# Kernel optimization log

Measured on AMD Instinct MI355X. Metric: run time of the kernel, lower is better.

## Reference

```python
import jax, jax.numpy as jnp
import numpy as np

D = 1024
H = 16
HD = D // H  # 64
LN_EPS = 1e-5


def _layernorm(x, w, b):
    m = jnp.mean(x, axis=-1, keepdims=True)
    v = jnp.mean(jnp.square(x - m), axis=-1, keepdims=True)
    return (x - m) * jax.lax.rsqrt(v + LN_EPS) * w + b


def _attention(x, w_qkv, b_qkv, w_proj, b_proj):
    # x: [B, S, D]. Block-diagonal mask == attention within each sequence,
    # so batched per-sequence attention is exactly equivalent to packed fmha.
    B, S, _ = x.shape
    qkv = x @ w_qkv + b_qkv                      # [B, S, 3D]
    q, k, v = jnp.split(qkv, 3, axis=-1)
    q = q.reshape(B, S, H, HD)
    k = k.reshape(B, S, H, HD)
    v = v.reshape(B, S, H, HD)
    scale = 1.0 / jnp.sqrt(jnp.asarray(HD, dtype=x.dtype))
    scores = jnp.einsum('bqhd,bkhd->bhqk', q, k) * scale  # [B, H, S, S]
    probs = jax.nn.softmax(scores, axis=-1)
    out = jnp.einsum('bhqk,bkhd->bqhd', probs, v).reshape(B, S, D)
    return out @ w_proj + b_proj


def _block(x, w_qkv, b_qkv, w_proj, b_proj, ln1_w, ln1_b,
           w_fc1, b_fc1, w_fc2, b_fc2, ln2_w, ln2_b, gamma1, gamma2):
    # x = x + ls1(attn(norm1(x)))
    x = x + gamma1 * _attention(_layernorm(x, ln1_w, ln1_b), w_qkv, b_qkv, w_proj, b_proj)
    # x = x + ls2(mlp(norm2(x)))
    h = _layernorm(x, ln2_w, ln2_b)
    h = jax.nn.gelu(h @ w_fc1 + b_fc1, approximate=False) @ w_fc2 + b_fc2
    return x + gamma2 * h


def setup_inputs() -> dict:
    key = jax.random.key(0)
    ks = jax.random.split(key, 8)
    s = 0.02
    return {
        'x1': jax.random.normal(ks[0], (8, 1024, D), jnp.float32),
        'x2': jax.random.normal(ks[1], (8, 512, D), jnp.float32),
        'w_qkv': jax.random.normal(ks[2], (D, 3 * D), jnp.float32) * s,
        'b_qkv': jnp.zeros((3 * D,), jnp.float32),
        'w_proj': jax.random.normal(ks[3], (D, D), jnp.float32) * s,
        'b_proj': jnp.zeros((D,), jnp.float32),
        'ln1_w': jnp.ones((D,), jnp.float32),
        'ln1_b': jnp.zeros((D,), jnp.float32),
        'ln2_w': jnp.ones((D,), jnp.float32),
        'ln2_b': jnp.zeros((D,), jnp.float32),
        'w_fc1': jax.random.normal(ks[4], (D, 4 * D), jnp.float32) * s,
        'b_fc1': jnp.zeros((4 * D,), jnp.float32),
        'w_fc2': jax.random.normal(ks[5], (4 * D, D), jnp.float32) * s,
        'b_fc2': jnp.zeros((D,), jnp.float32),
        'gamma1': jnp.full((D,), 1e-5, jnp.float32),  # LayerScale init_values
        'gamma2': jnp.full((D,), 1e-5, jnp.float32),
    }


def reference(x1, x2, w_qkv, b_qkv, w_proj, b_proj, ln1_w, ln1_b,
              ln2_w, ln2_b, w_fc1, b_fc1, w_fc2, b_fc2, gamma1, gamma2):
    params = (w_qkv, b_qkv, w_proj, b_proj, ln1_w, ln1_b,
              w_fc1, b_fc1, w_fc2, b_fc2, ln2_w, ln2_b, gamma1, gamma2)
    y1 = _block(x1, *params)
    y2 = _block(x2, *params)
    return (y1, y2)
```

## Files before the change

### kernel.cpp

```cpp
#include <hip/hip_runtime.h>
#include <cstddef>


typedef __bf16 b16x8 __attribute__((ext_vector_type(8)));
typedef float f32x4 __attribute__((ext_vector_type(4)));
typedef unsigned short u16x8 __attribute__((ext_vector_type(8)));
typedef unsigned short u16x4 __attribute__((ext_vector_type(4)));
typedef float f32x4v __attribute__((ext_vector_type(4)));

__device__ __forceinline__ unsigned short f2bf(float f) {
    unsigned int u = __builtin_bit_cast(unsigned int, f);
    return (unsigned short)((u + 0x7fffu + ((u >> 16) & 1u)) >> 16);
}
__device__ __forceinline__ unsigned short f2bf_trunc(float f) {
    return (unsigned short)(__builtin_bit_cast(unsigned int, f) >> 16);
}

__device__ __forceinline__ float exp2_f(float x) {
#if defined(__has_builtin)
#if __has_builtin(__builtin_amdgcn_exp2f)
    return __builtin_amdgcn_exp2f(x);
#else
    return exp2f(x);
#endif
#else
    return exp2f(x);
#endif
}

#define AS1C(p) ((const __attribute__((address_space(1))) void*)(p))
#define AS3(p)  ((__attribute__((address_space(3))) void*)(p))
#define FENCE() asm volatile("" ::: "memory")

__global__ __launch_bounds__(256) void wtrans_k(const float* __restrict__ in,
                                                unsigned short* __restrict__ out,
                                                int K, int N) {
    __shared__ float tile[32][33];
    int n0 = blockIdx.x << 5, k0 = blockIdx.y << 5;
    int tx = threadIdx.x & 31;
    int ty = threadIdx.x >> 5;
#pragma unroll
    for (int j = 0; j < 4; ++j)
        tile[ty + j * 8][tx] = in[(size_t)(k0 + ty + j * 8) * N + n0 + tx];
    __syncthreads();
#pragma unroll
    for (int j = 0; j < 4; ++j)
        out[(size_t)(n0 + ty + j * 8) * K + k0 + tx] = f2bf(tile[tx][ty + j * 8]);
}

__global__ __launch_bounds__(256) void vtrans_k(const unsigned short* __restrict__ qkv,
                                                unsigned short* __restrict__ vT) {
    __shared__ unsigned short tile[32][40];
    int tok0 = blockIdx.x << 5, c0 = blockIdx.y << 5;
    int tx = threadIdx.x & 31, ty = threadIdx.x >> 5;
#pragma unroll
    for (int j = 0; j < 4; ++j)
        tile[ty + j * 8][tx] = qkv[(size_t)(tok0 + ty + j * 8) * 3072 + 2048 + c0 + tx];
    __syncthreads();
#pragma unroll
    for (int j = 0; j < 4; ++j)
        vT[(size_t)(c0 + ty + j * 8) * 12288 + tok0 + tx] = tile[tx][ty + j * 8];
}

__global__ __launch_bounds__(256) void ln_k(const float* __restrict__ srcA,
                                            const float* __restrict__ srcB, int split,
                                            const float* __restrict__ w,
                                            const float* __restrict__ b,
                                            unsigned short* __restrict__ out) {
    int row = blockIdx.x;
    const float* src = (row < split) ? srcA + (size_t)row * 1024
                                     : srcB + (size_t)(row - split) * 1024;
    int t = threadIdx.x;
    f32x4v v = *(const f32x4v*)(src + t * 4);
    float s = v[0] + v[1] + v[2] + v[3];
    float s2 = v[0] * v[0] + v[1] * v[1] + v[2] * v[2] + v[3] * v[3];
#pragma unroll
    for (int off = 1; off < 64; off <<= 1) {
        s += __shfl_xor(s, off);
        s2 += __shfl_xor(s2, off);
    }
    __shared__ float red[8];
    int wv4 = t >> 6;
    if ((t & 63) == 0) { red[wv4 * 2] = s; red[wv4 * 2 + 1] = s2; }
    __syncthreads();
    s = red[0] + red[2] + red[4] + red[6];
    s2 = red[1] + red[3] + red[5] + red[7];
    float mean = s * (1.0f / 1024.0f);
    float var = s2 * (1.0f / 1024.0f) - mean * mean;
    float rstd = rsqrtf(var + 1e-5f);
    f32x4v wv = *(const f32x4v*)(w + t * 4);
    f32x4v bv = *(const f32x4v*)(b + t * 4);
    u16x4 ov;
#pragma unroll
    for (int j = 0; j < 4; ++j) ov[j] = f2bf((v[j] - mean) * rstd * wv[j] + bv[j]);
    *(u16x4*)(out + (size_t)row * 1024 + t * 4) = ov;
}

template <int BM, int K, int NN, int EPI>
__global__ __launch_bounds__(512, 1) void gemm3_k(
    const unsigned short* __restrict__ A, const unsigned short* __restrict__ BT,
    const float* __restrict__ bias, const float* __restrict__ scale,
    const float* __restrict__ rx1, const float* __restrict__ rx2,
    float* __restrict__ outf, unsigned short* __restrict__ outb) {
    constexpr int NT = K / 64;
    constexpr int ntn = NN >> 8;
    constexpr int GA = BM / 64;
    constexpr int NFR = BM / 32;
    constexpr int HALF = NFR / 2;
    constexpr int ABUF = BM * 128;
    constexpr int STRIDE = ABUF + 32768;
    __shared__ char lds[2 * STRIDE];
    const int t = threadIdx.x;
    const int lane = t & 63, w = t >> 6, lr = lane & 15, lg = lane >> 4;
    const int wm = w >> 2, wn = w & 3;
    const int nwg = gridDim.x;
    const int bid = blockIdx.x;
    const int swz = (bid & 7) * (nwg >> 3) + (bid >> 3);
    const int m0 = (swz / ntn) * BM;
    const int n0 = (swz % ntn) << 8;

    const int srow = t >> 3;
    const int scol = ((t & 7) ^ (srow & 7)) * 8;
    const unsigned short* ga = A + (size_t)(m0 + srow) * K + scol;
    const unsigned short* gb = BT + (size_t)(n0 + srow) * K + scol;

    f32x4 acc[NFR][4] = {};
    b16x8 af[HALF][2], b01[2][2], b23[2][2];

    auto ISSUE_A = [&](int tile, int g) {
        char* dst = lds + (tile & 1) * STRIDE + g * 8192 + t * 16;
        __builtin_amdgcn_global_load_lds(AS1C(ga + (size_t)(g * 64) * K + tile * 64),
                                         AS3(dst), 16, 0, 0);
    };
    auto ISSUE_B = [&](int tile, int g) {
        char* dst = lds + (tile & 1) * STRIDE + ABUF + g * 8192 + t * 16;
        __builtin_amdgcn_global_load_lds(AS1C(gb + (size_t)(g * 64) * K + tile * 64),
                                         AS3(dst), 16, 0, 0);
    };

    const int cs0 = (lg ^ (lr & 7)) * 16;
    const int cs1 = ((4 + lg) ^ (lr & 7)) * 16;

    auto RD_A = [&](const char* buf, int mg) {
#pragma unroll
        for (int mi = 0; mi < HALF; ++mi) {
            const char* p = buf + (wm * (BM / 2) + (mg + mi) * 16 + lr) * 128;
            af[mi][0] = *(const b16x8*)(p + cs0);
            af[mi][1] = *(const b16x8*)(p + cs1);
        }
    };
    auto RD_B = [&](const char* buf, b16x8 (*bf)[2], int ng) {
#pragma unroll
        for (int ni = 0; ni < 2; ++ni) {
            const char* p = buf + ABUF + (wn * 64 + (ng + ni) * 16 + lr) * 128;
            bf[ni][0] = *(const b16x8*)(p + cs0);
            bf[ni][1] = *(const b16x8*)(p + cs1);
        }
    };
    auto MM = [&](int mg, b16x8 (*bf)[2], int ng) {
        __builtin_amdgcn_s_setprio(1);
#pragma unroll
        for (int kk = 0; kk < 2; ++kk)
#pragma unroll
            for (int mi = 0; mi < HALF; ++mi)
#pragma unroll
                for (int ni = 0; ni < 2; ++ni)
                    acc[mg + mi][ng + ni] = __builtin_amdgcn_mfma_f32_16x16x32_bf16(
                        af[mi][kk], bf[ni][kk], acc[mg + mi][ng + ni], 0, 0, 0);
        __builtin_amdgcn_s_setprio(0);
    };
    auto WAIT_GA = [&]() {
        if constexpr (GA == 4) asm volatile("s_waitcnt vmcnt(4)" ::: "memory");
        else                   asm volatile("s_waitcnt vmcnt(3)" ::: "memory");
    };

#pragma unroll
    for (int g = 0; g < GA; ++g) ISSUE_A(0, g);
#pragma unroll
    for (int g = 0; g < 4; ++g) ISSUE_B(0, g);
#pragma unroll
    for (int g = 0; g < GA; ++g) ISSUE_A(1, g);
    WAIT_GA();
    __builtin_amdgcn_s_barrier();
    FENCE();

    for (int kt = 0; kt < NT; ++kt) {
        const char* buf = lds + (kt & 1) * STRIDE;
        RD_A(buf, 0); RD_B(buf, b01, 0);
        if (kt + 1 < NT) { ISSUE_B(kt + 1, 0); ISSUE_B(kt + 1, 1); }
        __builtin_amdgcn_s_barrier(); FENCE();
        MM(0, b01, 0);
        __builtin_amdgcn_s_barrier(); FENCE();
        RD_B(buf, b23, 2);
        if (kt + 1 < NT) { ISSUE_B(kt + 1, 2); ISSUE_B(kt + 1, 3); }
        __builtin_amdgcn_s_barrier(); FENCE();
        MM(0, b23, 2);
        __builtin_amdgcn_s_barrier(); FENCE();
        RD_A(buf, HALF);
        __builtin_amdgcn_s_barrier(); FENCE();
        MM(HALF, b23, 2);
        __builtin_amdgcn_s_barrier(); FENCE();
        if (kt + 2 < NT) {
#pragma unroll
            for (int g = 0; g < GA; ++g) ISSUE_A(kt + 2, g);
        }
        __builtin_amdgcn_s_barrier(); FENCE();
        MM(HALF, b01, 0);
        if (kt + 1 < NT) {
            if (kt + 2 < NT) WAIT_GA();
            else             asm volatile("s_waitcnt vmcnt(0)" ::: "memory");
            __builtin_amdgcn_s_barrier(); FENCE();
        }
    }

    if (EPI == 0 || EPI == 2) {
        __syncthreads();
        char* clb = lds;
        const int rl0 = wm * (BM / 2) + lg * 4;
        const int cl0 = wn * 64 + lr;
#pragma unroll
        for (int n = 0; n < 4; ++n) {
            const int col_l = cl0 + n * 16;
            const float bval = bias[n0 + col_l];
            const int colByte = col_l * 2;
            const int within = colByte & 15;
            const int chunk = colByte >> 4;
#pragma unroll
            for (int m = 0; m < NFR; ++m) {
#pragma unroll
                for (int r = 0; r < 4; ++r) {
                    float c = acc[m][n][r] + bval;
                    if (EPI == 2) {
                        float u = c * (c * c * 0.044715f + 1.0f) * 1.5957691216057308f;
                        c = c * __builtin_amdgcn_rcpf(1.0f + __expf(-u));
                    }
                    const int row_l = rl0 + m * 16 + r;
                    *(unsigned short*)(clb + row_l * 512 +
                                       (((chunk ^ (row_l & 7)) << 4) | within)) = f2bf(c);
                }
            }
        }
        __syncthreads();
#pragma unroll
        for (int it = 0; it < BM / 16; ++it) {
            int idx = it * 512 + t;
            int row = idx >> 5, ch = idx & 31;
            u16x8 v = *(const u16x8*)(clb + row * 512 + ((ch ^ (row & 7)) << 4));
            *(u16x8*)(outb + (size_t)(m0 + row) * NN + n0 + ch * 8) = v;
        }
    } else {
        const int rbase = m0 + wm * (BM / 2) + lg * 4;
        const int cbase = n0 + wn * 64 + lr;
#pragma unroll
        for (int n = 0; n < 4; ++n) {
            int col = cbase + n * 16;
            float bval = bias[col];
            float sval = scale[col];
#pragma unroll
            for (int m = 0; m < NFR; ++m) {
                int row = rbase + m * 16;
#pragma unroll
                for (int r = 0; r < 4; ++r) {
                    float c = acc[m][n][r] + bval;
                    size_t idx = (size_t)(row + r) * NN + col;
                    if (EPI == 1) {
                        float xv = (row + r < 8192) ? rx1[idx] : rx2[idx - (size_t)8192 * 1024];
                        outf[idx] = xv + sval * c;
                    } else {
                        outf[idx] += sval * c;
                    }
                }
            }
        }
    }
}

__global__ __launch_bounds__(512) void attn_k(const unsigned short* __restrict__ qkv,
                                              const unsigned short* __restrict__ vT,
                                              unsigned short* __restrict__ aout) {
    __shared__ char sK[2][8192];
    __shared__ char sV[2][8192];
    __shared__ unsigned short sP[8][16 * 72];
    int bid = (blockIdx.x & 7) * (gridDim.x >> 3) + (blockIdx.x >> 3);
    int t = threadIdx.x, lane = t & 63, w = t >> 6, lr = lane & 15, lg = lane >> 4;
    int seq0, S, h, qt;
    if (bid < 1024) {
        int b = bid >> 7, r = bid & 127;
        h = r >> 3; qt = r & 7; seq0 = b << 10; S = 1024;
    } else {
        int i2 = bid - 1024;
        int b = i2 >> 6, r = i2 & 63;
        h = r >> 2; qt = r & 3; seq0 = 8192 + (b << 9); S = 512;
    }
    int tok0 = seq0 + qt * 128;
    const size_t hoff = (size_t)h * 64;

    const int srow = t >> 3;
    const int sc = ((t & 7) ^ (srow & 7)) * 8;
    const unsigned short* kg = qkv + (size_t)(seq0 + srow) * 3072 + 1024 + hoff + sc;
    const unsigned short* vg = vT + (size_t)(hoff + srow) * 12288 + seq0 + sc;

    b16x8 aq0, aq1;
    {
        const unsigned short* qb = qkv + (size_t)(tok0 + w * 16 + lr) * 3072 + hoff;
        aq0 = *(const b16x8*)(qb + lg * 8);
        aq1 = *(const b16x8*)(qb + 32 + lg * 8);
    }

    auto STAGE = [&](int kt) {
        int slot = kt & 1;
        __builtin_amdgcn_global_load_lds(AS1C(kg + (size_t)(kt << 6) * 3072),
                                         AS3(sK[slot] + t * 16), 16, 0, 0);
        __builtin_amdgcn_global_load_lds(AS1C(vg + (kt << 6)),
                                         AS3(sV[slot] + t * 16), 16, 0, 0);
    };

    const int swz0 = (lg ^ (lr & 7)) * 16;
    const int swz1 = ((4 + lg) ^ (lr & 7)) * 16;
    const float SC = 0.18033688f;

    float m_run[4] = {-1e30f, -1e30f, -1e30f, -1e30f};
    float l_run[4] = {0.f, 0.f, 0.f, 0.f};
    f32x4 o[4] = {};
    unsigned short* sPw = sP[w];
    int nkv = S >> 6;

    STAGE(0);
    for (int kt = 0; kt < nkv; ++kt) {
        if (kt + 1 < nkv) {
            STAGE(kt + 1);
            asm volatile("s_waitcnt vmcnt(2)" ::: "memory");
        } else {
            asm volatile("s_waitcnt vmcnt(0)" ::: "memory");
        }
        __builtin_amdgcn_s_barrier();
        FENCE();
        const char* kb = sK[kt & 1];
        const char* vb = sV[kt & 1];
        f32x4 s[4];
#pragma unroll
        for (int n = 0; n < 4; ++n) {
            const char* kr = kb + (n * 16 + lr) * 128;
            b16x8 bk0 = *(const b16x8*)(kr + swz0);
            b16x8 bk1 = *(const b16x8*)(kr + swz1);
            f32x4 z = {};
            z = __builtin_amdgcn_mfma_f32_16x16x32_bf16(aq0, bk0, z, 0, 0, 0);
            z = __builtin_amdgcn_mfma_f32_16x16x32_bf16(aq1, bk1, z, 0, 0, 0);
            s[n] = z * SC;
        }
        float p[4][4];
#pragma unroll
        for (int r = 0; r < 4; ++r) {
            float tm = fmaxf(fmaxf(s[0][r], s[1][r]), fmaxf(s[2][r], s[3][r]));
            tm = fmaxf(tm, __shfl_xor(tm, 1));
            tm = fmaxf(tm, __shfl_xor(tm, 2));
            tm = fmaxf(tm, __shfl_xor(tm, 4));
            tm = fmaxf(tm, __shfl_xor(tm, 8));
            float mn = fmaxf(m_run[r], tm);
            float alpha = exp2_f(m_run[r] - mn);
            m_run[r] = mn;
            float rs = 0.f;
#pragma unroll
            for (int n = 0; n < 4; ++n) {
                float pv = exp2_f(s[n][r] - mn);
                p[n][r] = pv;
                rs += pv;
            }
            rs += __shfl_xor(rs, 1);
            rs += __shfl_xor(rs, 2);
            rs += __shfl_xor(rs, 4);
            rs += __shfl_xor(rs, 8);
            l_run[r] = l_run[r] * alpha + rs;
#pragma unroll
            for (int n = 0; n < 4; ++n) o[n][r] *= alpha;
        }
#pragma unroll
        for (int r = 0; r < 4; ++r)
#pragma unroll
            for (int n = 0; n < 4; ++n)
                sPw[(lg * 4 + r) * 72 + n * 16 + lr] = f2bf_trunc(p[n][r]);
        b16x8 ap0 = *(const b16x8*)(&sPw[lr * 72 + lg * 8]);
        b16x8 ap1 = *(const b16x8*)(&sPw[lr * 72 + 32 + lg * 8]);
#pragma unroll
        for (int n = 0; n < 4; ++n) {
            const char* vr = vb + (n * 16 + lr) * 128;
            b16x8 bv0 = *(const b16x8*)(vr + swz0);
            b16x8 bv1 = *(const b16x8*)(vr + swz1);
            o[n] = __builtin_amdgcn_mfma_f32_16x16x32_bf16(ap0, bv0, o[n], 0, 0, 0);
            o[n] = __builtin_amdgcn_mfma_f32_16x16x32_bf16(ap1, bv1, o[n], 0, 0, 0);
        }
        FENCE();
        if (kt + 1 < nkv) __builtin_amdgcn_s_barrier();
        FENCE();
    }
    __syncthreads();
    char* ob = sK[0];
#pragma unroll
    for (int r = 0; r < 4; ++r) {
        float inv = __builtin_amdgcn_rcpf(l_run[r]);
        const int row_l = w * 16 + lg * 4 + r;
#pragma unroll
        for (int n = 0; n < 4; ++n) {
            const int colByte = (n * 16 + lr) * 2;
            *(unsigned short*)(ob + row_l * 128 +
                               ((((colByte >> 4) ^ (row_l & 7)) << 4) | (colByte & 15))) =
                f2bf(o[n][r] * inv);
        }
    }
    __syncthreads();
#pragma unroll
    for (int it = 0; it < 2; ++it) {
        int idx = it * 512 + t;
        int row = idx >> 3, ch = idx & 7;
        u16x8 v = *(const u16x8*)(ob + row * 128 + ((ch ^ (row & 7)) << 4));
        *(u16x8*)(aout + (size_t)(tok0 + row) * 1024 + hoff + ch * 8) = v;
    }
}

extern "C" void kernel_launch(void* const* d_in, const int* in_sizes, int n_in,
                              void* d_out, int out_size, void* d_ws, size_t ws_size,
                              hipStream_t stream) {
    const float* x1     = (const float*)d_in[0];
    const float* x2     = (const float*)d_in[1];
    const float* w_qkv  = (const float*)d_in[2];
    const float* b_qkv  = (const float*)d_in[3];
    const float* w_proj = (const float*)d_in[4];
    const float* b_proj = (const float*)d_in[5];
    const float* ln1w   = (const float*)d_in[6];
    const float* ln1b   = (const float*)d_in[7];
    const float* ln2w   = (const float*)d_in[8];
    const float* ln2b   = (const float*)d_in[9];
    const float* w_fc1  = (const float*)d_in[10];
    const float* b_fc1  = (const float*)d_in[11];
    const float* w_fc2  = (const float*)d_in[12];
    const float* b_fc2  = (const float*)d_in[13];
    const float* gamma1 = (const float*)d_in[14];
    const float* gamma2 = (const float*)d_in[15];
    float* out = (float*)d_out;
    char* ws = (char*)d_ws;

    unsigned short* wqkvT  = (unsigned short*)(ws);
    unsigned short* wprojT = (unsigned short*)(ws + 6291456);
    unsigned short* wfc1T  = (unsigned short*)(ws + 8388608);
    unsigned short* wfc2T  = (unsigned short*)(ws + 16777216);
    unsigned short* lnbuf  = (unsigned short*)(ws + 25165824);
    unsigned short* qkvbuf = (unsigned short*)(ws + 50331648);
    unsigned short* attnbuf= (unsigned short*)(ws + 125829120);
    unsigned short* actbuf = (unsigned short*)(ws + 50331648);
    unsigned short* vTbuf  = lnbuf;

    wtrans_k<<<dim3(96, 32), 256, 0, stream>>>(w_qkv, wqkvT, 1024, 3072);
    wtrans_k<<<dim3(32, 32), 256, 0, stream>>>(w_proj, wprojT, 1024, 1024);
    wtrans_k<<<dim3(128, 32), 256, 0, stream>>>(w_fc1, wfc1T, 1024, 4096);
    wtrans_k<<<dim3(32, 128), 256, 0, stream>>>(w_fc2, wfc2T, 4096, 1024);
    ln_k<<<12288, 256, 0, stream>>>(x1, x2, 8192, ln1w, ln1b, lnbuf);
    gemm3_k<192, 1024, 3072, 0><<<768, 512, 0, stream>>>(lnbuf, wqkvT, b_qkv, nullptr,
                                                         nullptr, nullptr, nullptr, qkvbuf);
    vtrans_k<<<dim3(384, 32), 256, 0, stream>>>(qkvbuf, vTbuf);
    attn_k<<<1536, 512, 0, stream>>>(qkvbuf, vTbuf, attnbuf);
    gemm3_k<192, 1024, 1024, 1><<<256, 512, 0, stream>>>(attnbuf, wprojT, b_proj, gamma1,
                                                         x1, x2, out, nullptr);
    ln_k<<<12288, 256, 0, stream>>>(out, out + (size_t)8192 * 1024, 8192, ln2w, ln2b, lnbuf);
    gemm3_k<256, 1024, 4096, 2><<<768, 512, 0, stream>>>(lnbuf, wfc1T, b_fc1, nullptr,
                                                         nullptr, nullptr, nullptr, actbuf);
    gemm3_k<192, 4096, 1024, 3><<<256, 512, 0, stream>>>(actbuf, wfc2T, b_fc2, gamma2,
                                                         nullptr, nullptr, out, nullptr);
}
```

Measured before the change: 576.6 us.

## Load attention K/V fragments directly from global memory with smaller blocks

Attention no longer stages K and V tiles in double-buffered shared memory via global_load_lds with barriers. Each wave now reads its K and V MFMA fragments straight from global memory (relying on cache), and blocks shrink to 4 waves covering 64 query rows, with twice as many blocks. The XCD-interleaved block index remap is also dropped. This removes LDS staging and per-tile block barriers, but adds redundant global traffic across waves, poorly coalesced strided loads, and no explicit prefetch to hide load latency.

```diff
diff --git a/kernel.cpp b/kernel.cpp
--- a/kernel.cpp
+++ b/kernel.cpp
@@ -275,30 +275,23 @@
     }
 }
 
-__global__ __launch_bounds__(512) void attn_k(const unsigned short* __restrict__ qkv,
+__global__ __launch_bounds__(256) void attn_k(const unsigned short* __restrict__ qkv,
                                               const unsigned short* __restrict__ vT,
                                               unsigned short* __restrict__ aout) {
-    __shared__ char sK[2][8192];
-    __shared__ char sV[2][8192];
-    __shared__ unsigned short sP[8][16 * 72];
-    int bid = (blockIdx.x & 7) * (gridDim.x >> 3) + (blockIdx.x >> 3);
+    __shared__ unsigned short sP[4][16 * 72];
+    int bid = blockIdx.x;
     int t = threadIdx.x, lane = t & 63, w = t >> 6, lr = lane & 15, lg = lane >> 4;
     int seq0, S, h, qt;
-    if (bid < 1024) {
-        int b = bid >> 7, r = bid & 127;
-        h = r >> 3; qt = r & 7; seq0 = b << 10; S = 1024;
+    if (bid < 2048) {
+        int b = bid >> 8, r = bid & 255;
+        h = r >> 4; qt = r & 15; seq0 = b << 10; S = 1024;
     } else {
-        int i2 = bid - 1024;
-        int b = i2 >> 6, r = i2 & 63;
-        h = r >> 2; qt = r & 3; seq0 = 8192 + (b << 9); S = 512;
-    }
-    int tok0 = seq0 + qt * 128;
+        int i2 = bid - 2048;
+        int b = i2 >> 7, r = i2 & 127;
+        h = r >> 3; qt = r & 7; seq0 = 8192 + (b << 9); S = 512;
+    }
+    const int tok0 = bid < 2048 ? seq0 + qt * 64 : seq0 + qt * 64;
     const size_t hoff = (size_t)h * 64;
-
-    const int srow = t >> 3;
-    const int sc = ((t & 7) ^ (srow & 7)) * 8;
-    const unsigned short* kg = qkv + (size_t)(seq0 + srow) * 3072 + 1024 + hoff + sc;
-    const unsigned short* vg = vT + (size_t)(hoff + srow) * 12288 + seq0 + sc;
 
     b16x8 aq0, aq1;
     {
@@ -306,47 +299,35 @@
         aq0 = *(const b16x8*)(qb + lg * 8);
         aq1 = *(const b16x8*)(qb + 32 + lg * 8);
     }
-
-    auto STAGE = [&](int kt) {
-        int slot = kt & 1;
-        __builtin_amdgcn_global_load_lds(AS1C(kg + (size_t)(kt << 6) * 3072),
-                                         AS3(sK[slot] + t * 16), 16, 0, 0);
-        __builtin_amdgcn_global_load_lds(AS1C(vg + (kt << 6)),
-                                         AS3(sV[slot] + t * 16), 16, 0, 0);
-    };
-
-    const int swz0 = (lg ^ (lr & 7)) * 16;
-    const int swz1 = ((4 + lg) ^ (lr & 7)) * 16;
+    const unsigned short* kb = qkv + (size_t)seq0 * 3072 + 1024 + hoff + (size_t)(lr)*3072;
+    const unsigned short* vb = vT + (size_t)(hoff + lr) * 12288 + seq0;
+
     const float SC = 0.18033688f;
-
     float m_run[4] = {-1e30f, -1e30f, -1e30f, -1e30f};
     float l_run[4] = {0.f, 0.f, 0.f, 0.f};
     f32x4 o[4] = {};
     unsigned short* sPw = sP[w];
-    int nkv = S >> 6;
-
-    STAGE(0);
+    const int nkv = S >> 6;
+
     for (int kt = 0; kt < nkv; ++kt) {
-        if (kt + 1 < nkv) {
-            STAGE(kt + 1);
-            asm volatile("s_waitcnt vmcnt(2)" ::: "memory");
-        } else {
-            asm volatile("s_waitcnt vmcnt(0)" ::: "memory");
-        }
-        __builtin_amdgcn_s_barrier();
-        FENCE();
-        const char* kb = sK[kt & 1];
-        const char* vb = sV[kt & 1];
+        const int kv0 = kt << 6;
         f32x4 s[4];
 #pragma unroll
         for (int n = 0; n < 4; ++n) {
-            const char* kr = kb + (n * 16 + lr) * 128;
-            b16x8 bk0 = *(const b16x8*)(kr + swz0);
-            b16x8 bk1 = *(const b16x8*)(kr + swz1);
+            const unsigned short* kr = kb + (size_t)(kv0 + n * 16) * 3072;
+            b16x8 bk0 = *(const b16x8*)(kr + lg * 8);
+            b16x8 bk1 = *(const b16x8*)(kr + 32 + lg * 8);
             f32x4 z = {};
             z = __builtin_amdgcn_mfma_f32_16x16x32_bf16(aq0, bk0, z, 0, 0, 0);
             z = __builtin_amdgcn_mfma_f32_16x16x32_bf16(aq1, bk1, z, 0, 0, 0);
             s[n] = z * SC;
+        }
+        b16x8 bv0[4], bv1[4];
+#pragma unroll
+        for (int n = 0; n < 4; ++n) {
+            const unsigned short* vr = vb + (size_t)(n * 16) * 12288 + kv0;
+            bv0[n] = *(const b16x8*)(vr + lg * 8);
+            bv1[n] = *(const b16x8*)(vr + 32 + lg * 8);
         }
         float p[4][4];
 #pragma unroll
@@ -383,18 +364,12 @@
         b16x8 ap1 = *(const b16x8*)(&sPw[lr * 72 + 32 + lg * 8]);
 #pragma unroll
         for (int n = 0; n < 4; ++n) {
-            const char* vr = vb + (n * 16 + lr) * 128;
-            b16x8 bv0 = *(const b16x8*)(vr + swz0);
-            b16x8 bv1 = *(const b16x8*)(vr + swz1);
-            o[n] = __builtin_amdgcn_mfma_f32_16x16x32_bf16(ap0, bv0, o[n], 0, 0, 0);
-            o[n] = __builtin_amdgcn_mfma_f32_16x16x32_bf16(ap1, bv1, o[n], 0, 0, 0);
-        }
-        FENCE();
-        if (kt + 1 < nkv) __builtin_amdgcn_s_barrier();
-        FENCE();
+            o[n] = __builtin_amdgcn_mfma_f32_16x16x32_bf16(ap0, bv0[n], o[n], 0, 0, 0);
+            o[n] = __builtin_amdgcn_mfma_f32_16x16x32_bf16(ap1, bv1[n], o[n], 0, 0, 0);
+        }
     }
     __syncthreads();
-    char* ob = sK[0];
+    char* ob = (char*)sP;
 #pragma unroll
     for (int r = 0; r < 4; ++r) {
         float inv = __builtin_amdgcn_rcpf(l_run[r]);
@@ -410,7 +385,7 @@
     __syncthreads();
 #pragma unroll
     for (int it = 0; it < 2; ++it) {
-        int idx = it * 512 + t;
+        int idx = it * 256 + t;
         int row = idx >> 3, ch = idx & 7;
         u16x8 v = *(const u16x8*)(ob + row * 128 + ((ch ^ (row & 7)) << 4));
         *(u16x8*)(aout + (size_t)(tok0 + row) * 1024 + hoff + ch * 8) = v;
@@ -457,7 +432,7 @@
     gemm3_k<192, 1024, 3072, 0><<<768, 512, 0, stream>>>(lnbuf, wqkvT, b_qkv, nullptr,
                                                          nullptr, nullptr, nullptr, qkvbuf);
     vtrans_k<<<dim3(384, 32), 256, 0, stream>>>(qkvbuf, vTbuf);
-    attn_k<<<1536, 512, 0, stream>>>(qkvbuf, vTbuf, attnbuf);
+    attn_k<<<3072, 256, 0, stream>>>(qkvbuf, vTbuf, attnbuf);
     gemm3_k<192, 1024, 1024, 1><<<256, 512, 0, stream>>>(attnbuf, wprojT, b_proj, gamma1,
                                                          x1, x2, out, nullptr);
     ln_k<<<12288, 256, 0, stream>>>(out, out + (size_t)8192 * 1024, 8192, ln2w, ln2b, lnbuf);
```

New measurement: 723.2 us. +25.4%, slower.

## Software-pipeline attention so next-tile QK overlaps current PV, drop XCD block remap

Applied to the files above, without the earlier changes.

Restructures the attention inner loop so the QK^T MFMAs and softmax for the next KV tile are issued alongside the PV MFMAs of the current tile, with V fragments preloaded into registers. Loads for tile kt+2 are staged into the freed LDS slot after a mid-iteration barrier. The block-index remap that spread blocks across XCDs is also replaced by the plain block index. The aim is to hide softmax and LDS latency behind matrix work. The trade-offs are a full vmcnt(0) wait each iteration, which shortens how long the prefetch can overlap, plus higher register pressure and possibly worse L2 locality from the removed remap.

```diff
diff --git a/kernel.cpp b/kernel.cpp
--- a/kernel.cpp
+++ b/kernel.cpp
@@ -281,7 +281,7 @@
     __shared__ char sK[2][8192];
     __shared__ char sV[2][8192];
     __shared__ unsigned short sP[8][16 * 72];
-    int bid = (blockIdx.x & 7) * (gridDim.x >> 3) + (blockIdx.x >> 3);
+    int bid = blockIdx.x;
     int t = threadIdx.x, lane = t & 63, w = t >> 6, lr = lane & 15, lg = lane >> 4;
     int seq0, S, h, qt;
     if (bid < 1024) {
@@ -323,21 +323,10 @@
     float l_run[4] = {0.f, 0.f, 0.f, 0.f};
     f32x4 o[4] = {};
     unsigned short* sPw = sP[w];
-    int nkv = S >> 6;
-
-    STAGE(0);
-    for (int kt = 0; kt < nkv; ++kt) {
-        if (kt + 1 < nkv) {
-            STAGE(kt + 1);
-            asm volatile("s_waitcnt vmcnt(2)" ::: "memory");
-        } else {
-            asm volatile("s_waitcnt vmcnt(0)" ::: "memory");
-        }
-        __builtin_amdgcn_s_barrier();
-        FENCE();
+    const int nkv = S >> 6;
+
+    auto QK = [&](int kt, f32x4 (&s)[4]) {
         const char* kb = sK[kt & 1];
-        const char* vb = sV[kt & 1];
-        f32x4 s[4];
 #pragma unroll
         for (int n = 0; n < 4; ++n) {
             const char* kr = kb + (n * 16 + lr) * 128;
@@ -348,6 +337,8 @@
             z = __builtin_amdgcn_mfma_f32_16x16x32_bf16(aq1, bk1, z, 0, 0, 0);
             s[n] = z * SC;
         }
+    };
+    auto SM = [&](f32x4 (&s)[4], b16x8& a0, b16x8& a1) {
         float p[4][4];
 #pragma unroll
         for (int r = 0; r < 4; ++r) {
@@ -379,19 +370,46 @@
 #pragma unroll
             for (int n = 0; n < 4; ++n)
                 sPw[(lg * 4 + r) * 72 + n * 16 + lr] = f2bf_trunc(p[n][r]);
-        b16x8 ap0 = *(const b16x8*)(&sPw[lr * 72 + lg * 8]);
-        b16x8 ap1 = *(const b16x8*)(&sPw[lr * 72 + 32 + lg * 8]);
+        a0 = *(const b16x8*)(&sPw[lr * 72 + lg * 8]);
+        a1 = *(const b16x8*)(&sPw[lr * 72 + 32 + lg * 8]);
+    };
+
+    STAGE(0);
+    if (nkv > 1) STAGE(1);
+    asm volatile("s_waitcnt vmcnt(0)" ::: "memory");
+    __builtin_amdgcn_s_barrier();
+    FENCE();
+    f32x4 s0[4];
+    QK(0, s0);
+    b16x8 ap0, ap1;
+    SM(s0, ap0, ap1);
+
+    for (int kt = 0; kt < nkv; ++kt) {
+        const char* vb = sV[kt & 1];
+        b16x8 bv0[4], bv1[4];
 #pragma unroll
         for (int n = 0; n < 4; ++n) {
             const char* vr = vb + (n * 16 + lr) * 128;
-            b16x8 bv0 = *(const b16x8*)(vr + swz0);
-            b16x8 bv1 = *(const b16x8*)(vr + swz1);
-            o[n] = __builtin_amdgcn_mfma_f32_16x16x32_bf16(ap0, bv0, o[n], 0, 0, 0);
-            o[n] = __builtin_amdgcn_mfma_f32_16x16x32_bf16(ap1, bv1, o[n], 0, 0, 0);
-        }
+            bv0[n] = *(const b16x8*)(vr + swz0);
+            bv1[n] = *(const b16x8*)(vr + swz1);
+        }
+        f32x4 s2[4];
+        if (kt + 1 < nkv) QK(kt + 1, s2);
+        asm volatile("s_waitcnt lgkmcnt(0)" ::: "memory");
+        __builtin_amdgcn_s_barrier();
         FENCE();
-        if (kt + 1 < nkv) __builtin_amdgcn_s_barrier();
-        FENCE();
+        if (kt + 2 < nkv) STAGE(kt + 2);
+#pragma unroll
+        for (int n = 0; n < 4; ++n) {
+            o[n] = __builtin_amdgcn_mfma_f32_16x16x32_bf16(ap0, bv0[n], o[n], 0, 0, 0);
+            o[n] = __builtin_amdgcn_mfma_f32_16x16x32_bf16(ap1, bv1[n], o[n], 0, 0, 0);
+        }
+        if (kt + 1 < nkv) {
+            SM(s2, ap0, ap1);
+            asm volatile("s_waitcnt vmcnt(0)" ::: "memory");
+            __builtin_amdgcn_s_barrier();
+            FENCE();
+        }
     }
     __syncthreads();
     char* ob = sK[0];
```

New measurement: 557.4 us. 1.03x faster.
